# Optimization experiments

Hardware: AMD Instinct MI355X
Metric: run time of the kernel (lower is better)

The kernel has to match this reference:

```python
import jax, jax.numpy as jnp
import numpy as np

ALPHA = 0.5
INV_COEFF = 25.0
STD_COEFF = 25.0
COV_COEFF = 1.0
NUM_MATCHES = 50
EPS = 1e-5
GAMMA = 1.0


def _cdist(a, b):
    # (B,M,C),(B,N,C) -> (B,M,N) euclidean, matmul-based like torch.cdist
    a2 = jnp.sum(a * a, axis=-1, keepdims=True)            # (B,M,1)
    b2 = jnp.sum(b * b, axis=-1, keepdims=True)            # (B,N,1)
    d2 = a2 + jnp.swapaxes(b2, -1, -2) - 2.0 * jnp.einsum('bmc,bnc->bmn', a, b)
    return jnp.sqrt(jnp.maximum(d2, 0.0))


def _nn_match(input_maps, candidate_maps, distances, num_matches):
    # topk(k=1, largest=False) == min/argmin over last dim
    nn_dists = jnp.min(distances, axis=-1)                 # (B,M)
    nn_indices = jnp.argmin(distances, axis=-1)            # (B,M)
    # k smallest nn_dists, ascending order
    _, best_input_idx = jax.lax.top_k(-nn_dists, num_matches)   # (B,k)
    best_cand_idx = jnp.take_along_axis(nn_indices, best_input_idx, axis=1)
    filt_in = jnp.take_along_axis(input_maps, best_input_idx[:, :, None], axis=1)
    filt_cand = jnp.take_along_axis(candidate_maps, best_cand_idx[:, :, None], axis=1)
    return filt_in, filt_cand


def _off_diag_sq_sum(c):
    return jnp.sum(c * c) - jnp.sum(jnp.diag(c) ** 2)


def _std_term(x_flat):
    # unbiased variance over sample dim (torch var default)
    std = jnp.sqrt(jnp.var(x_flat, axis=0, ddof=1) + EPS)
    return jnp.mean(jax.nn.relu(GAMMA - std)) / 2.0


def _cov_term(x_flat):
    n, c = x_flat.shape
    xc = x_flat - jnp.mean(x_flat, axis=0)
    cov = xc.T @ xc / (n - 1)
    return _off_diag_sq_sum(cov) / c


def _vicreg_global(x, y):
    inv = jnp.mean((x - y) ** 2)
    std = _std_term(x) + _std_term(y)
    cov = _cov_term(x) + _cov_term(y)
    return INV_COEFF * inv + STD_COEFF * std + COV_COEFF * cov


def _vicregl_maps(x, y):
    # x, y: (B, k, C)
    inv = jnp.mean((x - y) ** 2)
    xf = x.reshape(-1, x.shape[-1])
    yf = y.reshape(-1, y.shape[-1])
    std = _std_term(xf) + _std_term(yf)
    cov = _cov_term(xf) + _cov_term(yf)
    return INV_COEFF * inv, STD_COEFF * std, COV_COEFF * cov


def _local_loss(spatial_1, spatial_2):
    B, C, H, W = spatial_1.shape
    maps_1 = spatial_1.reshape(B, C, H * W).transpose(0, 2, 1)   # (B,HW,C)
    maps_2 = spatial_2.reshape(B, C, H * W).transpose(0, 2, 1)
    d12 = _cdist(maps_1, maps_2)
    m1f, m1n = _nn_match(maps_1, maps_2, d12, NUM_MATCHES)
    d21 = _cdist(maps_2, maps_1)
    m2f, m2n = _nn_match(maps_2, maps_1, d21, NUM_MATCHES)
    inv1, var1, cov1 = _vicregl_maps(m1f, m1n)
    inv2, var2, cov2 = _vicregl_maps(m2f, m2n)
    return (inv1 + inv2) / 2 + (var1 + var2) / 2 + (cov1 + cov2) / 2


def setup_inputs() -> dict:
    key = jax.random.key(0)
    k1, k2, k3, k4 = jax.random.split(key, 4)
    B, C, H, W = 64, 768, 24, 24
    return {
        'spatial_1': jax.random.normal(k1, (B, C, H, W), dtype=jnp.float32),
        'pooled_1': jax.random.normal(k2, (B, C), dtype=jnp.float32),
        'spatial_2': jax.random.normal(k3, (B, C, H, W), dtype=jnp.float32),
        'pooled_2': jax.random.normal(k4, (B, C), dtype=jnp.float32),
    }


def reference(spatial_1, pooled_1, spatial_2, pooled_2):
    global_loss = _vicreg_global(pooled_1, pooled_2)
    local_loss = _local_loss(spatial_1, spatial_2)
    return ALPHA * global_loss + (1.0 - ALPHA) * local_loss
```

## Files before the change

kernel.cpp:

```cpp
#include <hip/hip_runtime.h>
#include <stdint.h>

typedef unsigned long long ull;
typedef unsigned int uint;
typedef unsigned short ushort;

typedef __attribute__((ext_vector_type(8))) short short8;
typedef __attribute__((ext_vector_type(4))) float floatx4;

#define B   64
#define C   768
#define HW  576
#define K   50
#define NLOC (B*K)

#define OFF_SLOTS   0
#define OFF_COLSUM  256
#define OFF_NN1     18688
#define OFF_NN2     313600
#define OFF_SELP    608512
#define OFF_SELQ    634112
#define OFF_NORM    659712
#define OFF_XT      954624
#define OFF_MP      OFF_XT
#define OFF_XGT     114200832
#define OFF_M       133861632

#define SLOT_INVG 0
#define SLOT_STD  1
#define SLOT_COV  7
#define SLOT_INV1 13
#define SLOT_INV2 14

__device__ __forceinline__ ull umin64(ull a, ull b) { return a < b ? a : b; }

__device__ __forceinline__ float bf2f_lo(uint u) { return __uint_as_float(u << 16); }
__device__ __forceinline__ float bf2f_hi(uint u) { return __uint_as_float(u & 0xffff0000u); }
__device__ __forceinline__ float bf2f(ushort u) { return __uint_as_float(((uint)u) << 16); }

__device__ __forceinline__ ushort f2bf(float f) {
    uint u = __float_as_uint(f);
    uint r = (u + 0x7fffu + ((u >> 16) & 1u)) >> 16;
    return (ushort)r;
}

__device__ __forceinline__ float blk_reduce_sum(float v, float* s4) {
    for (int off = 32; off > 0; off >>= 1) v += __shfl_down(v, off, 64);
    int lane = threadIdx.x & 63, w = threadIdx.x >> 6;
    if (lane == 0) s4[w] = v;
    __syncthreads();
    float r = 0.f;
    if (threadIdx.x == 0) r = s4[0] + s4[1] + s4[2] + s4[3];
    return r;
}

__global__ __launch_bounds__(256) void convert_kernel(const float* __restrict__ x1,
                                                      const float* __restrict__ x2,
                                                      ushort* __restrict__ xT,
                                                      float* __restrict__ norm) {
    int z = blockIdx.y;
    int which = z >> 6, b = z & 63;
    const float* X = (which ? x2 : x1) + (size_t)b * C * HW;
    int p0 = blockIdx.x * 64;
    int t = threadIdx.x;
    int cq = t & 15;
    int pq = t >> 4;
    const float* src = X + p0 + 4 * pq;
    ushort* dstb = xT + (((size_t)which * B + b) * HW + p0) * C;
    float ss[4] = {0.f, 0.f, 0.f, 0.f};

    floatx4 A[4], Bf[4];
#define LOADCH(dst, ch)                                                               \
    {                                                                                 \
        _Pragma("unroll") for (int i = 0; i < 4; ++i)                                 \
            dst[i] = *(const floatx4*)(src + (size_t)((ch) * 64 + 4 * cq + i) * HW);  \
    }
#define STORECH(sv, ch)                                                               \
    {                                                                                 \
        _Pragma("unroll") for (int j = 0; j < 4; ++j) {                               \
            ushort u0 = f2bf(sv[0][j]), u1 = f2bf(sv[1][j]);                          \
            ushort u2 = f2bf(sv[2][j]), u3 = f2bf(sv[3][j]);                          \
            uint2 wv;                                                                 \
            wv.x = (uint)u0 | ((uint)u1 << 16);                                       \
            wv.y = (uint)u2 | ((uint)u3 << 16);                                       \
            *(uint2*)(dstb + (size_t)(4 * pq + j) * C + (ch) * 64 + 4 * cq) = wv;     \
            float r0 = bf2f(u0), r1 = bf2f(u1), r2 = bf2f(u2), r3 = bf2f(u3);         \
            ss[j] = fmaf(r0, r0, ss[j]); ss[j] = fmaf(r1, r1, ss[j]);                 \
            ss[j] = fmaf(r2, r2, ss[j]); ss[j] = fmaf(r3, r3, ss[j]);                 \
        }                                                                             \
    }

    LOADCH(A, 0);
    for (int ch = 0; ch < 12; ch += 2) {
        LOADCH(Bf, ch + 1);
        STORECH(A, ch);
        if (ch + 2 < 12) LOADCH(A, ch + 2);
        STORECH(Bf, ch + 1);
    }
#undef LOADCH
#undef STORECH
#pragma unroll
    for (int j = 0; j < 4; ++j) {
        ss[j] += __shfl_xor(ss[j], 8, 16);
        ss[j] += __shfl_xor(ss[j], 4, 16);
        ss[j] += __shfl_xor(ss[j], 2, 16);
        ss[j] += __shfl_xor(ss[j], 1, 16);
    }
    float outv = (cq == 1) ? ss[1] : (cq == 2) ? ss[2] : (cq == 3) ? ss[3] : ss[0];
    if (cq < 4)
        norm[((size_t)which * B + b) * HW + p0 + 4 * pq + cq] = outv;
}

template<int NK>
__device__ __forceinline__ void gemm_pp(const ushort* (&gA)[2][2], const ushort* (&gB)[2][2],
                                        char* (&dA)[2][2], char* (&dB)[2][2],
                                        const char* As, const char* Bs,
                                        const int (&offA)[4], const int (&offB)[4],
                                        floatx4 (&acc)[4][4]) {
    auto issue = [&](int s, int k0) {
#pragma unroll
        for (int n = 0; n < 2; ++n) {
            __builtin_amdgcn_global_load_lds(
                (const __attribute__((address_space(1))) void*)(gA[s][n] + k0),
                (__attribute__((address_space(3))) void*)dA[s][n], 16, 0, 0);
            __builtin_amdgcn_global_load_lds(
                (const __attribute__((address_space(1))) void*)(gB[s][n] + k0),
                (__attribute__((address_space(3))) void*)dB[s][n], 16, 0, 0);
        }
    };
    auto compute = [&](int s) {
        short8 a[4], bb[4];
#pragma unroll
        for (int i = 0; i < 4; ++i) a[i] = *(const short8*)(As + s * 8192 + offA[i]);
#pragma unroll
        for (int j = 0; j < 4; ++j) bb[j] = *(const short8*)(Bs + s * 8192 + offB[j]);
#pragma unroll
        for (int i = 0; i < 4; ++i)
#pragma unroll
            for (int j = 0; j < 4; ++j)
                acc[i][j] = __builtin_amdgcn_mfma_f32_16x16x32_bf16(a[i], bb[j], acc[i][j], 0, 0, 0);
    };

    issue(0, 0);
    issue(1, 0);
    for (int k = 0; k < NK; ++k) {
        asm volatile("s_waitcnt vmcnt(4)" ::: "memory");
        __builtin_amdgcn_s_barrier();
        __builtin_amdgcn_sched_barrier(0);
        compute(0);
        __builtin_amdgcn_sched_barrier(0);
        __builtin_amdgcn_s_barrier();
        if (k + 1 < NK) {
            issue(0, (k + 1) * 64);
            asm volatile("s_waitcnt vmcnt(4)" ::: "memory");
        } else {
            asm volatile("s_waitcnt vmcnt(0)" ::: "memory");
        }
        __builtin_amdgcn_s_barrier();
        __builtin_amdgcn_sched_barrier(0);
        compute(1);
        __builtin_amdgcn_sched_barrier(0);
        __builtin_amdgcn_s_barrier();
        if (k + 1 < NK) issue(1, (k + 1) * 64);
    }
}

__global__ __launch_bounds__(256) void cdist_mfma(const ushort* __restrict__ xT,
                                                  const float* __restrict__ norm,
                                                  ull* __restrict__ nn1,
                                                  ull* __restrict__ nn2) {
    int id = blockIdx.x;
    int xcd = id & 7, slot = id >> 3;
    int b = xcd + 8 * (slot / 25);
    int t = slot % 25;
    int qt = t % 5, pt = t / 5;

    const ushort* X1 = xT + (size_t)b * HW * C;
    const ushort* X2 = xT + (size_t)(B + b) * HW * C;

    __shared__ ull pool[4224];
    char* As = (char*)pool;
    char* Bs = As + 16384;

    int tid = threadIdx.x;
    int w = tid >> 6, l = tid & 63;
    int quad = l >> 4, col = l & 15;
    int lrow = l >> 2, pos = l & 3;

    const ushort* gA[2][2]; const ushort* gB[2][2];
    char* dA[2][2]; char* dB[2][2];
#pragma unroll
    for (int n = 0; n < 2; ++n) {
        int sm = w * 32 + n * 16 + lrow;
        int cdat = pos ^ ((sm >> 1) & 3);
        int p = pt * 128 + sm; if (p >= HW) p = HW - 1;
        int q = qt * 128 + sm; if (q >= HW) q = HW - 1;
#pragma unroll
        for (int s = 0; s < 2; ++s) {
            gA[s][n] = X1 + (size_t)p * C + s * 32 + cdat * 8;
            gB[s][n] = X2 + (size_t)q * C + s * 32 + cdat * 8;
            dA[s][n] = As + s * 8192 + w * 2048 + n * 1024;
            dB[s][n] = Bs + s * 8192 + w * 2048 + n * 1024;
        }
    }

    int offA[4], offB[4];
#pragma unroll
    for (int i = 0; i < 4; ++i) {
        int m_loc = (w >> 1) * 64 + i * 16 + col;
        offA[i] = m_loc * 64 + ((quad ^ ((m_loc >> 1) & 3)) * 16);
        int n_loc = (w & 1) * 64 + i * 16 + col;
        offB[i] = n_loc * 64 + ((quad ^ ((n_loc >> 1) & 3)) * 16);
    }

    floatx4 zero = {0.f, 0.f, 0.f, 0.f};
    floatx4 acc[4][4];
#pragma unroll
    for (int i = 0; i < 4; ++i)
#pragma unroll
        for (int j = 0; j < 4; ++j) acc[i][j] = zero;

    gemm_pp<12>(gA, gB, dA, dB, As, Bs, offA, offB, acc);

    const float* n1g = norm + (size_t)b * HW;
    const float* n2g = norm + (size_t)(B + b) * HW;
    float n1v[4][4]; bool vp[4][4];
    float n2v[4];    bool vq[4];
#pragma unroll
    for (int i = 0; i < 4; ++i)
#pragma unroll
        for (int r = 0; r < 4; ++r) {
            int p = pt * 128 + (w >> 1) * 64 + i * 16 + quad * 4 + r;
            vp[i][r] = (p < HW);
            n1v[i][r] = n1g[p < HW ? p : (HW - 1)];
        }
#pragma unroll
    for (int j = 0; j < 4; ++j) {
        int q = qt * 128 + (w & 1) * 64 + j * 16 + col;
        vq[j] = (q < HW);
        n2v[j] = n2g[q < HW ? q : (HW - 1)];
    }

    __syncthreads();
    typedef ull row33[33];
    row33* red = (row33*)pool;

#pragma unroll
    for (int i = 0; i < 4; ++i)
#pragma unroll
        for (int r = 0; r < 4; ++r) {
            int p_loc = (w >> 1) * 64 + i * 16 + quad * 4 + r;
            ull best = ~0ull;
#pragma unroll
            for (int j = 0; j < 4; ++j) {
                if (!vq[j]) continue;
                float d2 = fmaxf(n1v[i][r] + n2v[j] - 2.0f * acc[i][j][r], 0.0f);
                unsigned q_glob = qt * 128 + (w & 1) * 64 + j * 16 + col;
                best = umin64(best, ((ull)__float_as_uint(d2) << 32) | q_glob);
            }
            red[p_loc][(w & 1) * 16 + col] = best;
        }
    __syncthreads();
    if (tid < 128) {
        int p_glob = pt * 128 + tid;
        ull m = ~0ull;
#pragma unroll
        for (int x = 0; x < 32; ++x) m = umin64(m, red[tid][x]);
        if (p_glob < HW) atomicMin(&nn1[(size_t)b * HW + p_glob], m);
    }
    __syncthreads();
#pragma unroll
    for (int j = 0; j < 4; ++j) {
        int q_loc = (w & 1) * 64 + j * 16 + col;
        ull best = ~0ull;
#pragma unroll
        for (int i = 0; i < 4; ++i)
#pragma unroll
            for (int r = 0; r < 4; ++r) {
                if (!vp[i][r]) continue;
                float d2 = fmaxf(n1v[i][r] + n2v[j] - 2.0f * acc[i][j][r], 0.0f);
                unsigned p_glob = pt * 128 + (w >> 1) * 64 + i * 16 + quad * 4 + r;
                best = umin64(best, ((ull)__float_as_uint(d2) << 32) | p_glob);
            }
        red[q_loc][(w >> 1) * 4 + quad] = best;
    }
    __syncthreads();
    if (tid < 128) {
        int q_glob = qt * 128 + tid;
        ull m = ~0ull;
#pragma unroll
        for (int x = 0; x < 8; ++x) m = umin64(m, red[tid][x]);
        if (q_glob < HW) atomicMin(&nn2[(size_t)b * HW + q_glob], m);
    }
}

__global__ __launch_bounds__(64) void select_topk_wave(const ull* __restrict__ nn1,
                                                       const ull* __restrict__ nn2,
                                                       int* __restrict__ sel_p,
                                                       int* __restrict__ sel_q) {
    int b = blockIdx.x, dir = blockIdx.y;
    const ull* nn = dir ? nn2 : nn1;
    int lane = threadIdx.x;
    ull key[9]; uint qv[9];
#pragma unroll
    for (int r = 0; r < 9; ++r) {
        int p = r * 64 + lane;
        ull e = nn[(size_t)b * HW + p];
        key[r] = (e & 0xFFFFFFFF00000000ull) | (unsigned)p;
        qv[r] = (uint)(e & 0xFFFFFFFFu);
    }
    int* sp = sel_p + (dir * B + b) * K;
    int* sq = sel_q + (dir * B + b) * K;
    for (int it = 0; it < K; ++it) {
        ull m = key[0];
#pragma unroll
        for (int r = 1; r < 9; ++r) m = umin64(m, key[r]);
#pragma unroll
        for (int off = 32; off > 0; off >>= 1) m = umin64(m, __shfl_xor(m, off, 64));
#pragma unroll
        for (int r = 0; r < 9; ++r) {
            if (key[r] == m) {
                sp[it] = (int)(uint)(m & 0xFFFFFFFFu);
                sq[it] = (int)qv[r];
                key[r] = ~0ull;
            }
        }
    }
}

__global__ __launch_bounds__(256) void gather_jmajor(const ushort* __restrict__ xT,
                                                     const int* __restrict__ sel_p,
                                                     const int* __restrict__ sel_q,
                                                     ushort* __restrict__ XgT) {
    int j = blockIdx.x, s = blockIdx.y;
    int dir = s >> 1;
    int whichsrc = (s == 1 || s == 2) ? 1 : 0;
    const int* sel = (s & 1) ? sel_q : sel_p;
    __shared__ int sidx[64];
    __shared__ uint buf[64][33];
    int tid = threadIdx.x;
    if (tid < 64) sidx[tid] = sel[(dir * B + tid) * K + j];
    __syncthreads();
    int rb = tid >> 2, u = tid & 3;
    const ushort* srow = xT + (((size_t)whichsrc * B + rb) * HW + sidx[rb]) * C;
    int wv = tid >> 6, lb = tid & 63;
    ushort* obase = XgT + (size_t)s * C * NLOC + (size_t)j * 64 + lb;
    for (int ch = 0; ch < 12; ++ch) {
        __syncthreads();
        uint4 v0 = *(const uint4*)(srow + ch * 64 + u * 8);
        uint4 v1 = *(const uint4*)(srow + ch * 64 + (u + 4) * 8);
        buf[rb][u * 4 + 0] = v0.x; buf[rb][u * 4 + 1] = v0.y;
        buf[rb][u * 4 + 2] = v0.z; buf[rb][u * 4 + 3] = v0.w;
        buf[rb][(u + 4) * 4 + 0] = v1.x; buf[rb][(u + 4) * 4 + 1] = v1.y;
        buf[rb][(u + 4) * 4 + 2] = v1.z; buf[rb][(u + 4) * 4 + 3] = v1.w;
        __syncthreads();
#pragma unroll
        for (int st = 0; st < 16; ++st) {
            int cl = wv + st * 4;
            uint uv = buf[lb][cl >> 1];
            ushort val = (cl & 1) ? (ushort)(uv >> 16) : (ushort)(uv & 0xffffu);
            obase[(size_t)(ch * 64 + cl) * NLOC] = val;
        }
    }
}

__global__ __launch_bounds__(256) void ata_mfma(const ushort* __restrict__ XgT,
                                                float* __restrict__ Mp) {
    int bx = blockIdx.x;
    int mat = blockIdx.y, split = blockIdx.z;
    int rt = bx / 6, ct = bx % 6;
    const ushort* X = XgT + (size_t)mat * C * NLOC;

    __shared__ ull pool[4096];
    char* As = (char*)pool;
    char* Bs = As + 16384;

    int tid = threadIdx.x;
    int w = tid >> 6, l = tid & 63;
    int quad = l >> 4, col = l & 15;
    int lrow = l >> 2, pos = l & 3;

    const ushort* gA[2][2]; const ushort* gB[2][2];
    char* dA[2][2]; char* dB[2][2];
#pragma unroll
    for (int n = 0; n < 2; ++n) {
        int sm = w * 32 + n * 16 + lrow;
        int cdat = pos ^ ((sm >> 1) & 3);
#pragma unroll
        for (int s = 0; s < 2; ++s) {
            gA[s][n] = X + (size_t)(rt * 128 + sm) * NLOC + split * 640 + s * 32 + cdat * 8;
            gB[s][n] = X + (size_t)(ct * 128 + sm) * NLOC + split * 640 + s * 32 + cdat * 8;
            dA[s][n] = As + s * 8192 + w * 2048 + n * 1024;
            dB[s][n] = Bs + s * 8192 + w * 2048 + n * 1024;
        }
    }

    int offA[4], offB[4];
#pragma unroll
    for (int i = 0; i < 4; ++i) {
        int m_loc = (w >> 1) * 64 + i * 16 + col;
        offA[i] = m_loc * 64 + ((quad ^ ((m_loc >> 1) & 3)) * 16);
        int n_loc = (w & 1) * 64 + i * 16 + col;
        offB[i] = n_loc * 64 + ((quad ^ ((n_loc >> 1) & 3)) * 16);
    }

    floatx4 zero = {0.f, 0.f, 0.f, 0.f};
    floatx4 acc[4][4];
#pragma unroll
    for (int i = 0; i < 4; ++i)
#pragma unroll
        for (int j = 0; j < 4; ++j) acc[i][j] = zero;

    gemm_pp<10>(gA, gB, dA, dB, As, Bs, offA, offB, acc);

    float* Mo = Mp + (size_t)(mat * 5 + split) * C * C;
#pragma unroll
    for (int i = 0; i < 4; ++i)
#pragma unroll
        for (int j = 0; j < 4; ++j)
#pragma unroll
            for (int r = 0; r < 4; ++r) {
                int row = rt * 128 + (w >> 1) * 64 + i * 16 + quad * 4 + r;
                int cc  = ct * 128 + (w & 1) * 64 + j * 16 + col;
                Mo[(size_t)row * C + cc] = acc[i][j][r];
            }
}

__global__ __launch_bounds__(256) void reduce_mp(const float* __restrict__ Mp,
                                                 float* __restrict__ M) {
    int mat = blockIdx.y;
    int i = blockIdx.x * 256 + threadIdx.x;
    float4 r = {0.f, 0.f, 0.f, 0.f};
#pragma unroll
    for (int s = 0; s < 5; ++s) {
        const float4* a = (const float4*)(Mp + (size_t)(mat * 5 + s) * C * C);
        float4 v = a[i];
        r.x += v.x; r.y += v.y; r.z += v.z; r.w += v.w;
    }
    ((float4*)(M + (size_t)mat * C * C))[i] = r;
}

__global__ __launch_bounds__(256) void ata_pooled(const float* __restrict__ p1,
                                                  const float* __restrict__ p2,
                                                  float* __restrict__ M) {
    int mat = 4 + blockIdx.z;
    const float* X = (mat == 4) ? p1 : p2;
    int n = B;
    float* Mo = M + (size_t)mat * C * C;
    int ct = blockIdx.x, rt = blockIdx.y;

    __shared__ float As[16][64];
    __shared__ float Bs[16][64];
    int tid = threadIdx.x;
    int tx = tid & 15, ty = tid >> 4;
    int lr = tid >> 4, lc = (tid & 15) * 4;

    float acc[4][4] = {};
    for (int k0 = 0; k0 < n; k0 += 16) {
        float4 av = *(const float4*)&X[(size_t)(k0 + lr) * C + rt * 64 + lc];
        float4 bv = *(const float4*)&X[(size_t)(k0 + lr) * C + ct * 64 + lc];
        __syncthreads();
        *(float4*)&As[lr][lc] = av;
        *(float4*)&Bs[lr][lc] = bv;
        __syncthreads();
#pragma unroll
        for (int kk = 0; kk < 16; ++kk) {
            float4 af = *(const float4*)&As[kk][ty * 4];
            float4 bf = *(const float4*)&Bs[kk][tx * 4];
            float a[4] = {af.x, af.y, af.z, af.w};
            float bb[4] = {bf.x, bf.y, bf.z, bf.w};
#pragma unroll
            for (int i = 0; i < 4; ++i)
#pragma unroll
                for (int j = 0; j < 4; ++j)
                    acc[i][j] = fmaf(a[i], bb[j], acc[i][j]);
        }
    }
#pragma unroll
    for (int i = 0; i < 4; ++i) {
        float4 o = {acc[i][0], acc[i][1], acc[i][2], acc[i][3]};
        *(float4*)&Mo[(size_t)(rt * 64 + ty * 4 + i) * C + ct * 64 + tx * 4] = o;
    }
}

__global__ __launch_bounds__(256) void colsum4_kernel(const ushort* __restrict__ XgT,
                                                      float* __restrict__ colsum) {
    int mat = blockIdx.y, cb = blockIdx.x * 4;
    int r = threadIdx.x >> 6, lane = threadIdx.x & 63;
    const ushort* row = XgT + ((size_t)mat * C + cb + r) * NLOC;
    float s = 0.f;
    for (int i = lane; i < NLOC; i += 64) s += bf2f(row[i]);
    for (int off = 32; off > 0; off >>= 1) s += __shfl_down(s, off, 64);
    if (lane == 0) colsum[mat * C + cb + r] = s;
}

__global__ __launch_bounds__(256) void colsum_pooled(const float* __restrict__ p1,
                                                     const float* __restrict__ p2,
                                                     float* __restrict__ colsum) {
    int mat = 4 + blockIdx.y;
    const float* X = (mat == 4) ? p1 : p2;
    int c = blockIdx.x * 256 + threadIdx.x;
    float s = 0.f;
    for (int r = 0; r < B; ++r) s += X[(size_t)r * C + c];
    colsum[mat * C + c] = s;
}

__global__ __launch_bounds__(256) void std_kernel(const float* __restrict__ M,
                                                  const float* __restrict__ colsum,
                                                  float* __restrict__ slots) {
    int mat = blockIdx.y;
    float n = (mat < 4) ? (float)NLOC : (float)B;
    int c = blockIdx.x * 256 + threadIdx.x;
    float r = 0.f;
    if (c < C) {
        float mcc = M[(size_t)mat * C * C + (size_t)c * C + c];
        float cs = colsum[mat * C + c];
        float var = (mcc - cs * cs / n) / (n - 1.0f);
        float sd = sqrtf(var + 1e-5f);
        float g = 1.0f - sd;
        r = g > 0.f ? g : 0.f;
    }
    __shared__ float s4[4];
    float t = blk_reduce_sum(r, s4);
    if (threadIdx.x == 0) atomicAdd(&slots[SLOT_STD + mat], t);
}

__global__ __launch_bounds__(256) void cov_kernel(const float* __restrict__ M,
                                                  const float* __restrict__ colsum,
                                                  float* __restrict__ slots) {
    int mat = blockIdx.y;
    float n = (mat < 4) ? (float)NLOC : (float)B;
    float invn1 = 1.0f / (n - 1.0f);
    const float* Mm = M + (size_t)mat * C * C;
    __shared__ float cs_s[C];
    for (int c = threadIdx.x; c < C; c += 256) cs_s[c] = colsum[mat * C + c];
    __syncthreads();
    float s = 0.f;
    int r0 = blockIdx.x * 16;
    for (int r = 0; r < 16; ++r) {
        int row = r0 + r;
        float csr = cs_s[row] / n;
        const float* Mr = Mm + (size_t)row * C;
        for (int c = threadIdx.x; c < C; c += 256) {
            float cv = (Mr[c] - csr * cs_s[c]) * invn1;
            if (c != row) s = fmaf(cv, cv, s);
        }
    }
    __shared__ float s4[4];
    float t = blk_reduce_sum(s, s4);
    if (threadIdx.x == 0) atomicAdd(&slots[SLOT_COV + mat], t);
}

__global__ __launch_bounds__(256) void inv_global_kernel(const float* __restrict__ p1,
                                                         const float* __restrict__ p2,
                                                         float* __restrict__ slots) {
    int idx = blockIdx.x * 256 + threadIdx.x;
    int stride = gridDim.x * 256;
    float s = 0.f;
    for (int i = idx; i < B * C; i += stride) {
        float d = p1[i] - p2[i];
        s = fmaf(d, d, s);
    }
    __shared__ float s4[4];
    float t = blk_reduce_sum(s, s4);
    if (threadIdx.x == 0) atomicAdd(&slots[SLOT_INVG], t);
}

__global__ __launch_bounds__(256) void inv_local2(const ushort* __restrict__ XgT,
                                                  float* __restrict__ slots) {
    int pair = blockIdx.y;
    const uint* A4 = (const uint*)(XgT + (size_t)(2 * pair) * C * NLOC);
    const uint* B4 = (const uint*)(XgT + (size_t)(2 * pair + 1) * C * NLOC);
    int idx = blockIdx.x * 256 + threadIdx.x;
    int stride = gridDim.x * 256;
    int n = C * NLOC / 2;
    float s = 0.f;
    for (int i = idx; i < n; i += stride) {
        uint ua = A4[i], ub = B4[i];
        float d0 = bf2f_lo(ua) - bf2f_lo(ub);
        float d1 = bf2f_hi(ua) - bf2f_hi(ub);
        s = fmaf(d0, d0, s);
        s = fmaf(d1, d1, s);
    }
    __shared__ float s4[4];
    float t = blk_reduce_sum(s, s4);
    if (threadIdx.x == 0) atomicAdd(&slots[(pair == 0) ? SLOT_INV1 : SLOT_INV2], t);
}

__global__ void final_kernel(const float* __restrict__ slots, float* __restrict__ out) {
    float std_t[6], cov_t[6];
    for (int m = 0; m < 6; ++m) {
        std_t[m] = slots[SLOT_STD + m] / (float)C * 0.5f;
        cov_t[m] = slots[SLOT_COV + m] / (float)C;
    }
    float inv_g = slots[SLOT_INVG] / (float)(B * C);
    float global_loss = 25.0f * inv_g + 25.0f * (std_t[4] + std_t[5]) + (cov_t[4] + cov_t[5]);
    float inv1 = 25.0f * slots[SLOT_INV1] / (float)(NLOC * C);
    float inv2 = 25.0f * slots[SLOT_INV2] / (float)(NLOC * C);
    float var1 = 25.0f * (std_t[0] + std_t[1]);
    float var2 = 25.0f * (std_t[2] + std_t[3]);
    float cov1 = cov_t[0] + cov_t[1];
    float cov2 = cov_t[2] + cov_t[3];
    float local_loss = (inv1 + inv2) * 0.5f + (var1 + var2) * 0.5f + (cov1 + cov2) * 0.5f;
    out[0] = 0.5f * global_loss + 0.5f * local_loss;
}

extern "C" void kernel_launch(void* const* d_in, const int* in_sizes, int n_in,
                              void* d_out, int out_size, void* d_ws, size_t ws_size,
                              hipStream_t stream) {
    const float* spatial_1 = (const float*)d_in[0];
    const float* pooled_1  = (const float*)d_in[1];
    const float* spatial_2 = (const float*)d_in[2];
    const float* pooled_2  = (const float*)d_in[3];
    float* out = (float*)d_out;

    char* ws = (char*)d_ws;
    float*  slots  = (float*)(ws + OFF_SLOTS);
    float*  colsum = (float*)(ws + OFF_COLSUM);
    ull*    nn1    = (ull*)(ws + OFF_NN1);
    ull*    nn2    = (ull*)(ws + OFF_NN2);
    int*    sel_p  = (int*)(ws + OFF_SELP);
    int*    sel_q  = (int*)(ws + OFF_SELQ);
    float*  norm   = (float*)(ws + OFF_NORM);
    ushort* xT     = (ushort*)(ws + OFF_XT);
    float*  Mp     = (float*)(ws + OFF_MP);
    ushort* XgT    = (ushort*)(ws + OFF_XGT);
    float*  M      = (float*)(ws + OFF_M);

    hipMemsetAsync(ws, 0, OFF_NN1, stream);
    hipMemsetAsync(ws + OFF_NN1, 0xFF, OFF_SELP - OFF_NN1, stream);

    convert_kernel<<<dim3(9, 128), 256, 0, stream>>>(spatial_1, spatial_2, xT, norm);
    cdist_mfma<<<1600, 256, 0, stream>>>(xT, norm, nn1, nn2);
    select_topk_wave<<<dim3(B, 2), 64, 0, stream>>>(nn1, nn2, sel_p, sel_q);
    gather_jmajor<<<dim3(K, 4), 256, 0, stream>>>(xT, sel_p, sel_q, XgT);
    ata_mfma<<<dim3(36, 4, 5), 256, 0, stream>>>(XgT, Mp);
    ata_pooled<<<dim3(12, 12, 2), 256, 0, stream>>>(pooled_1, pooled_2, M);
    reduce_mp<<<dim3(576, 4), 256, 0, stream>>>(Mp, M);
    colsum4_kernel<<<dim3(192, 4), 256, 0, stream>>>(XgT, colsum);
    colsum_pooled<<<dim3(3, 2), 256, 0, stream>>>(pooled_1, pooled_2, colsum);
    std_kernel<<<dim3(3, 6), 256, 0, stream>>>(M, colsum, slots);
    cov_kernel<<<dim3(48, 6), 256, 0, stream>>>(M, colsum, slots);
    inv_global_kernel<<<dim3(96), 256, 0, stream>>>(pooled_1, pooled_2, slots);
    inv_local2<<<dim3(300, 2), 256, 0, stream>>>(XgT, slots);
    final_kernel<<<1, 1, 0, stream>>>(slots, out);
}
```

Measured before the change: 479.9 us.

## Stage transpose through LDS and split channels across two blocks per tile

The fp32-to-bf16 transpose kernel now stages each 64-position by 384-channel tile in shared memory and writes fully coalesced 16-byte rows to the transposed buffer, where it previously did scattered 8-byte stores. Each position tile is split into two channel halves, which doubles the grid. Each half writes a partial squared norm to a buffer placed at the M workspace region, and cdist sums the two partials when it loads them. This adds LDS traffic and a barrier, and it relies on M not being written before cdist has read the partial norms.

```diff
diff --git a/kernel.cpp b/kernel.cpp
--- a/kernel.cpp
+++ b/kernel.cpp
@@ -57,58 +57,64 @@
 __global__ __launch_bounds__(256) void convert_kernel(const float* __restrict__ x1,
                                                       const float* __restrict__ x2,
                                                       ushort* __restrict__ xT,
-                                                      float* __restrict__ norm) {
+                                                      float* __restrict__ normp) {
     int z = blockIdx.y;
     int which = z >> 6, b = z & 63;
-    const float* X = (which ? x2 : x1) + (size_t)b * C * HW;
-    int p0 = blockIdx.x * 64;
+    int half = blockIdx.x & 1;
+    int pt = blockIdx.x >> 1;
+    int p0 = pt * 64, c0 = half * 384;
+    const float* X = (which ? x2 : x1) + ((size_t)b * C + c0) * HW + p0;
+
+    __shared__ ushort tile[64][392];
+    __shared__ float nlds[64][4];
+
     int t = threadIdx.x;
-    int cq = t & 15;
-    int pq = t >> 4;
-    const float* src = X + p0 + 4 * pq;
-    ushort* dstb = xT + (((size_t)which * B + b) * HW + p0) * C;
+    int pq = t & 15, cq = t >> 4;
+    int w = t >> 6;
+
     float ss[4] = {0.f, 0.f, 0.f, 0.f};
 
-    floatx4 A[4], Bf[4];
-#define LOADCH(dst, ch)                                                               \
-    {                                                                                 \
-        _Pragma("unroll") for (int i = 0; i < 4; ++i)                                 \
-            dst[i] = *(const floatx4*)(src + (size_t)((ch) * 64 + 4 * cq + i) * HW);  \
-    }
-#define STORECH(sv, ch)                                                               \
-    {                                                                                 \
-        _Pragma("unroll") for (int j = 0; j < 4; ++j) {                               \
-            ushort u0 = f2bf(sv[0][j]), u1 = f2bf(sv[1][j]);                          \
-            ushort u2 = f2bf(sv[2][j]), u3 = f2bf(sv[3][j]);                          \
-            uint2 wv;                                                                 \
-            wv.x = (uint)u0 | ((uint)u1 << 16);                                       \
-            wv.y = (uint)u2 | ((uint)u3 << 16);                                       \
-            *(uint2*)(dstb + (size_t)(4 * pq + j) * C + (ch) * 64 + 4 * cq) = wv;     \
-            float r0 = bf2f(u0), r1 = bf2f(u1), r2 = bf2f(u2), r3 = bf2f(u3);         \
-            ss[j] = fmaf(r0, r0, ss[j]); ss[j] = fmaf(r1, r1, ss[j]);                 \
-            ss[j] = fmaf(r2, r2, ss[j]); ss[j] = fmaf(r3, r3, ss[j]);                 \
-        }                                                                             \
-    }
-
-    LOADCH(A, 0);
-    for (int ch = 0; ch < 12; ch += 2) {
-        LOADCH(Bf, ch + 1);
-        STORECH(A, ch);
-        if (ch + 2 < 12) LOADCH(A, ch + 2);
-        STORECH(Bf, ch + 1);
-    }
-#undef LOADCH
-#undef STORECH
+#pragma unroll
+    for (int pass = 0; pass < 6; ++pass) {
+        floatx4 v[4];
+#pragma unroll
+        for (int i = 0; i < 4; ++i)
+            v[i] = *(const floatx4*)(X + (size_t)(pass * 64 + 4 * cq + i) * HW + 4 * pq);
+#pragma unroll
+        for (int j = 0; j < 4; ++j) {
+            ushort u0 = f2bf(v[0][j]), u1 = f2bf(v[1][j]);
+            ushort u2 = f2bf(v[2][j]), u3 = f2bf(v[3][j]);
+            ushort4 uu; uu.x = u0; uu.y = u1; uu.z = u2; uu.w = u3;
+            *(ushort4*)&tile[4 * pq + j][pass * 64 + 4 * cq] = uu;
+            float r0 = bf2f(u0), r1 = bf2f(u1), r2 = bf2f(u2), r3 = bf2f(u3);
+            ss[j] = fmaf(r0, r0, ss[j]); ss[j] = fmaf(r1, r1, ss[j]);
+            ss[j] = fmaf(r2, r2, ss[j]); ss[j] = fmaf(r3, r3, ss[j]);
+        }
+    }
 #pragma unroll
     for (int j = 0; j < 4; ++j) {
-        ss[j] += __shfl_xor(ss[j], 8, 16);
-        ss[j] += __shfl_xor(ss[j], 4, 16);
-        ss[j] += __shfl_xor(ss[j], 2, 16);
-        ss[j] += __shfl_xor(ss[j], 1, 16);
-    }
-    float outv = (cq == 1) ? ss[1] : (cq == 2) ? ss[2] : (cq == 3) ? ss[3] : ss[0];
-    if (cq < 4)
-        norm[((size_t)which * B + b) * HW + p0 + 4 * pq + cq] = outv;
+        ss[j] += __shfl_xor(ss[j], 16, 64);
+        ss[j] += __shfl_xor(ss[j], 32, 64);
+    }
+    if ((t & 63) < 16) {
+#pragma unroll
+        for (int j = 0; j < 4; ++j) nlds[4 * pq + j][w] = ss[j];
+    }
+    __syncthreads();
+
+    ushort* dst = xT + (((size_t)which * B + b) * HW + p0) * C + c0;
+    const char* tb = (const char*)tile;
+#pragma unroll
+    for (int step = 0; step < 12; ++step) {
+        int ib = (step * 256 + t) * 16;
+        int p = ib / 768, cb = ib % 768;
+        short8 vv = *(const short8*)(tb + (size_t)p * 784 + cb);
+        *(short8*)(dst + (size_t)p * C + (cb >> 1)) = vv;
+    }
+    if (t < 64) {
+        float nv = nlds[t][0] + nlds[t][1] + nlds[t][2] + nlds[t][3];
+        normp[((size_t)half * 128 + which * 64 + b) * HW + p0 + t] = nv;
+    }
 }
 
 template<int NK>
@@ -166,7 +172,7 @@
 }
 
 __global__ __launch_bounds__(256) void cdist_mfma(const ushort* __restrict__ xT,
-                                                  const float* __restrict__ norm,
+                                                  const float* __restrict__ normp,
                                                   ull* __restrict__ nn1,
                                                   ull* __restrict__ nn2) {
     int id = blockIdx.x;
@@ -222,8 +228,10 @@
 
     gemm_pp<12>(gA, gB, dA, dB, As, Bs, offA, offB, acc);
 
-    const float* n1g = norm + (size_t)b * HW;
-    const float* n2g = norm + (size_t)(B + b) * HW;
+    const float* n1a = normp + (size_t)b * HW;
+    const float* n1b = normp + (size_t)(128 + b) * HW;
+    const float* n2a = normp + (size_t)(64 + b) * HW;
+    const float* n2b = normp + (size_t)(192 + b) * HW;
     float n1v[4][4]; bool vp[4][4];
     float n2v[4];    bool vq[4];
 #pragma unroll
@@ -232,13 +240,15 @@
         for (int r = 0; r < 4; ++r) {
             int p = pt * 128 + (w >> 1) * 64 + i * 16 + quad * 4 + r;
             vp[i][r] = (p < HW);
-            n1v[i][r] = n1g[p < HW ? p : (HW - 1)];
+            int pc = p < HW ? p : (HW - 1);
+            n1v[i][r] = n1a[pc] + n1b[pc];
         }
 #pragma unroll
     for (int j = 0; j < 4; ++j) {
         int q = qt * 128 + (w & 1) * 64 + j * 16 + col;
         vq[j] = (q < HW);
-        n2v[j] = n2g[q < HW ? q : (HW - 1)];
+        int qc = q < HW ? q : (HW - 1);
+        n2v[j] = n2a[qc] + n2b[qc];
     }
 
     __syncthreads();
@@ -621,17 +631,17 @@
     ull*    nn2    = (ull*)(ws + OFF_NN2);
     int*    sel_p  = (int*)(ws + OFF_SELP);
     int*    sel_q  = (int*)(ws + OFF_SELQ);
-    float*  norm   = (float*)(ws + OFF_NORM);
     ushort* xT     = (ushort*)(ws + OFF_XT);
     float*  Mp     = (float*)(ws + OFF_MP);
     ushort* XgT    = (ushort*)(ws + OFF_XGT);
     float*  M      = (float*)(ws + OFF_M);
+    float*  normp  = (float*)(ws + OFF_M);
 
     hipMemsetAsync(ws, 0, OFF_NN1, stream);
     hipMemsetAsync(ws + OFF_NN1, 0xFF, OFF_SELP - OFF_NN1, stream);
 
-    convert_kernel<<<dim3(9, 128), 256, 0, stream>>>(spatial_1, spatial_2, xT, norm);
-    cdist_mfma<<<1600, 256, 0, stream>>>(xT, norm, nn1, nn2);
+    convert_kernel<<<dim3(18, 128), 256, 0, stream>>>(spatial_1, spatial_2, xT, normp);
+    cdist_mfma<<<1600, 256, 0, stream>>>(xT, normp, nn1, nn2);
     select_topk_wave<<<dim3(B, 2), 64, 0, stream>>>(nn1, nn2, sel_p, sel_q);
     gather_jmajor<<<dim3(K, 4), 256, 0, stream>>>(xT, sel_p, sel_q, XgT);
     ata_mfma<<<dim3(36, 4, 5), 256, 0, stream>>>(XgT, Mp);
```

Result: no change. 472.9 us (-1.5%).
